# Optimization experiments

Measured on AMD Instinct MI355X. Metric: run time of the kernel, lower is better.

Reference implementation:

```python
import jax, jax.numpy as jnp
import numpy as np

B, H, W, C = 8, 56, 56, 384
HEADS = 12
HD = C // HEADS          # 32 head dim
WS = 7                   # window size
SS = 3                   # shift size
N = WS * WS              # 49 tokens per window
HID = int(C * 4.0)       # 1536 mlp hidden
NW = (H // WS) * (W // WS)  # 64 windows per image
EPS = 1e-5


def _relative_position_index(ws):
    coords = np.stack(np.meshgrid(np.arange(ws), np.arange(ws), indexing='ij'))
    cf = coords.reshape(2, -1)
    rel = (cf[:, :, None] - cf[:, None, :]).transpose(1, 2, 0)
    rel[:, :, 0] += ws - 1
    rel[:, :, 1] += ws - 1
    rel[:, :, 0] *= 2 * ws - 1
    return rel.sum(-1).astype(np.int32)  # [N, N]

REL_IDX = _relative_position_index(WS)


def _swin_shift_mask(hh, ww, ws, ss):
    # standard Swin shift mask: label 9 regions, windows with mixed labels get -100
    img = np.zeros((hh, ww), dtype=np.float32)
    cnt = 0
    for hs in (slice(0, -ws), slice(-ws, -ss), slice(-ss, None)):
        for wsl in (slice(0, -ws), slice(-ws, -ss), slice(-ss, None)):
            img[hs, wsl] = cnt
            cnt += 1
    wins = img.reshape(hh // ws, ws, ww // ws, ws).transpose(0, 2, 1, 3).reshape(-1, ws * ws)
    diff = wins[:, None, :] - wins[:, :, None]
    return np.where(diff != 0, -100.0, 0.0).astype(np.float32)  # [nW, N, N]


def setup_inputs() -> dict:
    key = jax.random.key(0)
    ks = jax.random.split(key, 8)
    s = 0.02
    return {
        'x': jax.random.normal(ks[0], (B, H, W, C), jnp.float32),
        'attention_mask': jnp.asarray(_swin_shift_mask(H, W, WS, SS)),
        'qkv_w': jax.random.normal(ks[1], (C, 3 * C), jnp.float32) * s,
        'qkv_b': jnp.zeros((3 * C,), jnp.float32),
        'proj_w': jax.random.normal(ks[2], (C, C), jnp.float32) * s,
        'proj_b': jnp.zeros((C,), jnp.float32),
        'rpb_table': jax.random.normal(ks[3], ((2 * WS - 1) * (2 * WS - 1), HEADS), jnp.float32) * s,
        'norm1_g': jnp.ones((C,), jnp.float32),
        'norm1_b': jnp.zeros((C,), jnp.float32),
        'norm2_g': jnp.ones((C,), jnp.float32),
        'norm2_b': jnp.zeros((C,), jnp.float32),
        'fc1_w': jax.random.normal(ks[4], (C, HID), jnp.float32) * s,
        'fc1_b': jnp.zeros((HID,), jnp.float32),
        'fc2_w': jax.random.normal(ks[5], (HID, C), jnp.float32) * s,
        'fc2_b': jnp.zeros((C,), jnp.float32),
    }


def _ln(x, g, b):
    mu = jnp.mean(x, axis=-1, keepdims=True)
    var = jnp.mean(jnp.square(x - mu), axis=-1, keepdims=True)
    return (x - mu) / jnp.sqrt(var + EPS) * g + b


def reference(x, attention_mask, qkv_w, qkv_b, proj_w, proj_b, rpb_table,
              norm1_g, norm1_b, norm2_g, norm2_b, fc1_w, fc1_b, fc2_w, fc2_b):
    b = x.shape[0]
    nh, nw = H // WS, W // WS
    shortcut = x.reshape(b, H * W, C)

    h = _ln(x, norm1_g, norm1_b)
    # cyclic shift (H,W divisible by WS -> no padding needed)
    h = jnp.roll(h, (-SS, -SS), axis=(1, 2))
    # window partition -> [b*nW, N, C]
    win = h.reshape(b, nh, WS, nw, WS, C).transpose(0, 1, 3, 2, 4, 5).reshape(-1, N, C)

    qkv = (win @ qkv_w + qkv_b).reshape(-1, N, 3, HEADS, HD).transpose(2, 0, 3, 1, 4)
    q, k, v = qkv[0] * (HD ** -0.5), qkv[1], qkv[2]  # each [b*nW, heads, N, HD]

    attn = jnp.einsum('bhnd,bhmd->bhnm', q, k)  # [b*nW, heads, N, N]
    bias = rpb_table[REL_IDX.reshape(-1)].reshape(N, N, HEADS).transpose(2, 0, 1)
    attn = attn + bias[None]
    # additive shift mask per window
    attn = attn.reshape(b, NW, HEADS, N, N) + attention_mask[None, :, None]
    attn = jax.nn.softmax(attn.reshape(-1, HEADS, N, N), axis=-1)

    out = jnp.einsum('bhnm,bhmd->bhnd', attn, v).transpose(0, 2, 1, 3).reshape(-1, N, C)
    out = out @ proj_w + proj_b
    # window reverse
    out = out.reshape(b, nh, nw, WS, WS, C).transpose(0, 1, 3, 2, 4, 5).reshape(b, H, W, C)
    out = jnp.roll(out, (SS, SS), axis=(1, 2)).reshape(b, H * W, C)

    xr = shortcut + out
    m = _ln(xr.reshape(b, H * W, C), norm2_g, norm2_b)
    m = jax.nn.gelu(m @ fc1_w + fc1_b, approximate=False) @ fc2_w + fc2_b
    xr = xr + m
    return xr.reshape(b, H, W, C)
```

## Files before the change

### kernel.cpp

```cpp
#include <hip/hip_runtime.h>
#include <hip/hip_bf16.h>
#include <math.h>

#define BD 8
#define HH 56
#define WW 56
#define CC 384
#define HEADS 12
#define HD 32
#define WS 7
#define SS 3
#define NTOK 49
#define NWIN 64
#define TOKENS (BD*HH*WW)
#define HID 1536
#define TPI (HH*WW)

typedef __attribute__((ext_vector_type(8))) short bf16x8;
typedef __attribute__((ext_vector_type(4))) float f32x4;

__device__ __forceinline__ unsigned short f2bf(float f) {
    unsigned int u = __float_as_uint(f);
    unsigned int r = (u + 0x7FFFu + ((u >> 16) & 1u)) >> 16;
    return (unsigned short)r;
}
__device__ __forceinline__ unsigned short f2bf_fast(float v) {
    unsigned int w;
    asm("v_cvt_pk_bf16_f32 %0, %1, %2" : "=v"(w) : "v"(v), "v"(v));
    return (unsigned short)w;
}
__device__ __forceinline__ float bf2f(unsigned short h) {
    return __uint_as_float(((unsigned int)h) << 16);
}
__device__ __forceinline__ void gload16(const void* g, void* l) {
    __builtin_amdgcn_global_load_lds((const __attribute__((address_space(1))) unsigned int*)g,
                                     (__attribute__((address_space(3))) unsigned int*)l, 16, 0, 0);
}
__device__ __forceinline__ float fgelu(float x) {
    float x2 = x * x;
    float y  = x * fmaf(0.03567740814f, x2, 0.7978845608f);
    float e  = exp2f(y * 2.8853900818f);
    float r  = __builtin_amdgcn_rcpf(e + 1.0f);
    return x - x * r;
}
__device__ __forceinline__ int xcd_swz(int lid, int nwg) {
    int xcd = lid & 7, pos = lid >> 3;
    int q = nwg >> 3, r = nwg & 7;
    return (xcd < r ? xcd * (q + 1) : r * (q + 1) + (xcd - r) * q) + pos;
}

__global__ __launch_bounds__(256)
void wprep(const float* __restrict__ W, unsigned short* __restrict__ Th, int K, int N)
{
    __shared__ float t[32][33];
    int n0 = blockIdx.x * 32, k0 = blockIdx.y * 32;
    int c = threadIdx.x & 31, r = threadIdx.x >> 5;
    #pragma unroll
    for (int rr = 0; rr < 32; rr += 8)
        t[r + rr][c] = W[(size_t)(k0 + r + rr) * N + n0 + c];
    __syncthreads();
    #pragma unroll
    for (int rr = 0; rr < 32; rr += 8) {
        int i = r + rr;
        Th[(size_t)(n0 + i) * K + k0 + c] = f2bf(t[c][i]);
    }
}

__global__ __launch_bounds__(256)
void bias_prep(const float* __restrict__ rpb, float* __restrict__ Bias)
{
    int e = blockIdx.x * 256 + threadIdx.x;
    int wtq = e / 49152;
    int hr  = e - wtq * 49152;
    int h   = hr >> 12;
    int rem = hr & 4095;
    int jt = rem >> 10, it = (rem >> 8) & 3, lane = (rem >> 2) & 63, reg = rem & 3;
    int j = jt * 16 + ((lane >> 4) << 2) + reg;
    int i = it * 16 + (lane & 15);
    float val;
    if (j >= NTOK) val = -1e30f;
    else if (i >= NTOK) val = 0.0f;
    else {
        int ti = i / 7, tj = i - ti * 7, yj = j / 7, xj = j - yj * 7;
        float b = rpb[((ti - yj + 6) * 13 + (tj - xj + 6)) * HEADS + h];
        int wh7 = wtq >> 1, ww7 = wtq & 1;
        int lhi = wh7 ? (ti < 4 ? 1 : 2) : 0, lhj = wh7 ? (yj < 4 ? 1 : 2) : 0;
        int lwi = ww7 ? (tj < 4 ? 1 : 2) : 0, lwj = ww7 ? (xj < 4 ? 1 : 2) : 0;
        if (lhi != lhj || lwi != lwj) b -= 100.0f;
        val = b * 5.65685424949238f;
    }
    Bias[e] = val;
}

template<bool SHIFT>
__global__ __launch_bounds__(128)
void ln_kernel(const float* __restrict__ in, const float* __restrict__ g,
               const float* __restrict__ beta, unsigned short* __restrict__ oh)
{
    int m = blockIdx.x;
    const float* src;
    size_t dbase = (size_t)m * CC;
    if (SHIFT) {
        int b  = m / (NWIN * NTOK);
        int rr = m % (NWIN * NTOK);
        int w  = rr / NTOK;
        int t  = rr % NTOK;
        int wh = w >> 3, ww = w & 7;
        int ti = t / 7,  tj = t - (t / 7) * 7;
        int hh = wh * WS + ti + SS;  if (hh >= HH) hh -= HH;
        int w2 = ww * WS + tj + SS;  if (w2 >= WW) w2 -= WW;
        src = in + ((size_t)b * TPI + hh * WW + w2) * CC;
    } else {
        src = in + (size_t)m * CC;
    }
    int tid = threadIdx.x;
    float v0 = src[tid], v1 = src[tid + 128], v2 = src[tid + 256];
    float s  = v0 + v1 + v2;
    float ss = v0*v0 + v1*v1 + v2*v2;
    #pragma unroll
    for (int off = 32; off > 0; off >>= 1) {
        s  += __shfl_down(s, off);
        ss += __shfl_down(ss, off);
    }
    __shared__ float red[4];
    int wid = tid >> 6, lane = tid & 63;
    if (lane == 0) { red[wid] = s; red[wid + 2] = ss; }
    __syncthreads();
    float tot   = red[0] + red[1];
    float totss = red[2] + red[3];
    float mu   = tot * (1.0f / CC);
    float var  = totss * (1.0f / CC) - mu * mu;
    float rstd = rsqrtf(var + 1e-5f);
    #pragma unroll
    for (int e = 0; e < 3; ++e) {
        int idx = tid + e * 128;
        float v = (e == 0 ? v0 : (e == 1 ? v1 : v2));
        float y = (v - mu) * rstd * g[idx] + beta[idx];
        oh[dbase + idx] = f2bf_fast(y);
    }
}

#define EPI_QKV  0
#define EPI_GELU 1
#define EPI_PROJ 2
#define EPI_FC2  3

#define COMPUTE128(B) do {                                                          \
    bf16x8 ah[4], bh[2];                                                            \
    _Pragma("unroll")                                                               \
    for (int f = 0; f < 4; ++f) {                                                   \
        int row = wr * 64 + f * 16 + rA;                                            \
        int pp = (kslot ^ ((row >> 1) & 3)) * 8;                                    \
        ah[f] = *(const bf16x8*)&lds[B][0][row][pp];                                \
    }                                                                               \
    _Pragma("unroll")                                                               \
    for (int f = 0; f < 2; ++f) {                                                   \
        int col = wc * 32 + f * 16 + rA;                                            \
        int pb = (kslot ^ ((col >> 1) & 3)) * 8;                                    \
        bh[f] = *(const bf16x8*)&lds[B][1][col][pb];                                \
    }                                                                               \
    _Pragma("unroll")                                                               \
    for (int i = 0; i < 4; ++i)                                                     \
        _Pragma("unroll")                                                           \
        for (int j = 0; j < 2; ++j)                                                 \
            acc[i][j] = __builtin_amdgcn_mfma_f32_16x16x32_bf16(ah[i], bh[j], acc[i][j], 0, 0, 0); \
} while (0)

template<int EPI>
__global__ __launch_bounds__(512)
void gemm_mfma(const unsigned short* __restrict__ Ah, const unsigned short* __restrict__ Bh,
               const float* __restrict__ bias, const float* __restrict__ extra,
               float* __restrict__ outf, unsigned short* __restrict__ outh,
               int M, int N, int K)
{
    __shared__ unsigned short lds[3][2][128][32];

    int nwg = gridDim.x * gridDim.y;
    int wid = xcd_swz(blockIdx.y * gridDim.x + blockIdx.x, nwg);
    int nblk = wid % gridDim.x;
    int mblk = wid / gridDim.x;

    int tid  = threadIdx.x;
    int lane = tid & 63;
    int wave = tid >> 6;
    int wr = wave >> 2;
    int wc = wave & 3;
    int m0 = mblk * 128, n0 = nblk * 128;

    int lrow = lane >> 2;
    int ps   = lane & 3;
    int kslot = lane >> 4;
    int rA    = lane & 15;

    const unsigned short* gsrc[2];
    unsigned short* d0[2];
    unsigned short* d1[2];
    unsigned short* d2[2];
    #pragma unroll
    for (int s = 0; s < 2; ++s) {
        int seg = wave * 2 + s;
        int bf = seg >> 3, c = seg & 7;
        const unsigned short* gb = (bf == 0) ? Ah : Bh;
        int r0 = (bf == 0) ? m0 : n0;
        int row = c * 16 + lrow;
        int ks = ps ^ ((row >> 1) & 3);
        gsrc[s] = gb + (size_t)(r0 + row) * K + ks * 8;
        d0[s] = &lds[0][bf][c * 16][0];
        d1[s] = &lds[1][bf][c * 16][0];
        d2[s] = &lds[2][bf][c * 16][0];
    }

    f32x4 acc[4][2];
    #pragma unroll
    for (int i = 0; i < 4; ++i)
        #pragma unroll
        for (int j = 0; j < 2; ++j)
            acc[i][j] = (f32x4){0.f, 0.f, 0.f, 0.f};

    const int nt = K / 32;
    gload16(gsrc[0], d0[0]);
    gload16(gsrc[1], d0[1]);
    gload16(gsrc[0] + 32, d1[0]);
    gload16(gsrc[1] + 32, d1[1]);
    for (int t = 0; t < nt; t += 3) {
        if (t + 2 < nt) {
            int ka = (t + 2) * 32;
            gload16(gsrc[0] + ka, d2[0]);
            gload16(gsrc[1] + ka, d2[1]);
            asm volatile("s_waitcnt vmcnt(4)" ::: "memory");
        } else if (t + 1 < nt) {
            asm volatile("s_waitcnt vmcnt(2)" ::: "memory");
        } else {
            asm volatile("s_waitcnt vmcnt(0)" ::: "memory");
        }
        __builtin_amdgcn_sched_barrier(0);
        __builtin_amdgcn_s_barrier();
        __builtin_amdgcn_sched_barrier(0);
        COMPUTE128(0);
        __builtin_amdgcn_s_barrier();
        if (t + 3 < nt) {
            int kb = (t + 3) * 32;
            gload16(gsrc[0] + kb, d0[0]);
            gload16(gsrc[1] + kb, d0[1]);
            asm volatile("s_waitcnt vmcnt(4)" ::: "memory");
        } else if (t + 2 < nt) {
            asm volatile("s_waitcnt vmcnt(2)" ::: "memory");
        } else {
            asm volatile("s_waitcnt vmcnt(0)" ::: "memory");
        }
        __builtin_amdgcn_sched_barrier(0);
        __builtin_amdgcn_s_barrier();
        __builtin_amdgcn_sched_barrier(0);
        COMPUTE128(1);
        __builtin_amdgcn_s_barrier();
        if (t + 4 < nt) {
            int kc = (t + 4) * 32;
            gload16(gsrc[0] + kc, d1[0]);
            gload16(gsrc[1] + kc, d1[1]);
            asm volatile("s_waitcnt vmcnt(4)" ::: "memory");
        } else if (t + 3 < nt) {
            asm volatile("s_waitcnt vmcnt(2)" ::: "memory");
        } else {
            asm volatile("s_waitcnt vmcnt(0)" ::: "memory");
        }
        __builtin_amdgcn_sched_barrier(0);
        __builtin_amdgcn_s_barrier();
        __builtin_amdgcn_sched_barrier(0);
        COMPUTE128(2);
        __builtin_amdgcn_s_barrier();
    }

    int cn = lane & 15;
    int rb = (lane >> 4) * 4;
    float bj[2];
    #pragma unroll
    for (int j = 0; j < 2; ++j) bj[j] = bias[n0 + wc * 32 + j * 16 + cn];
    int ncol = n0 + wc * 32 + cn;

    #pragma unroll
    for (int i = 0; i < 4; ++i) {
        #pragma unroll
        for (int r = 0; r < 4; ++r) {
            int mg = m0 + wr * 64 + i * 16 + rb + r;
            if (EPI == EPI_PROJ) {
                int b  = mg / (NWIN * NTOK);
                int rr = mg % (NWIN * NTOK);
                int w  = rr / NTOK;
                int t  = rr % NTOK;
                int wh = w >> 3, ww = w & 7;
                int ti = t / 7,  tj = t - (t / 7) * 7;
                int hh = wh * WS + ti + SS;  if (hh >= HH) hh -= HH;
                int w2 = ww * WS + tj + SS;  if (w2 >= WW) w2 -= WW;
                size_t pix = (size_t)b * TPI + hh * WW + w2;
                const float* xin = extra + pix * CC + ncol;
                float* xo = outf + pix * CC + ncol;
                #pragma unroll
                for (int j = 0; j < 2; ++j) xo[j * 16] = xin[j * 16] + acc[i][j][r] + bj[j];
            } else {
                const float* xi = extra + (size_t)mg * N + ncol;
                float* xo = outf + (size_t)mg * N + ncol;
                #pragma unroll
                for (int j = 0; j < 2; ++j) xo[j * 16] = xi[j * 16] + acc[i][j][r] + bj[j];
            }
        }
    }
}

#define COMPUTE256(B) do {                                                          \
    bf16x8 ah[4], bh[4];                                                            \
    _Pragma("unroll")                                                               \
    for (int f = 0; f < 4; ++f) {                                                   \
        int row = wr * 64 + f * 16 + rA;                                            \
        int pp = (kslot ^ ((row >> 1) & 3)) * 8;                                    \
        ah[f] = *(const bf16x8*)&ldsA[B][row][pp];                                  \
        int col = wc * 64 + f * 16 + rA;                                            \
        int pb = (kslot ^ ((col >> 1) & 3)) * 8;                                    \
        bh[f] = *(const bf16x8*)&ldsB[B][col][pb];                                  \
    }                                                                               \
    _Pragma("unroll")                                                               \
    for (int i = 0; i < 4; ++i)                                                     \
        _Pragma("unroll")                                                           \
        for (int j = 0; j < 4; ++j)                                                 \
            acc[i][j] = __builtin_amdgcn_mfma_f32_16x16x32_bf16(ah[i], bh[j], acc[i][j], 0, 0, 0); \
} while (0)

template<int EPI>
__global__ __launch_bounds__(512)
void gemm_mfma256(const unsigned short* __restrict__ Ah, const unsigned short* __restrict__ Bh,
                  const float* __restrict__ bias,
                  float* __restrict__ outf, unsigned short* __restrict__ outh,
                  int M, int N, int K)
{
    __shared__ unsigned short ldsA[2][256][32];
    __shared__ unsigned short ldsB[2][128][32];

    int nwg = gridDim.x * gridDim.y;
    int wid = xcd_swz(blockIdx.y * gridDim.x + blockIdx.x, nwg);
    int nblk = wid % gridDim.x;
    int mblk = wid / gridDim.x;

    int tid  = threadIdx.x;
    int lane = tid & 63;
    int wave = tid >> 6;
    int wr = wave >> 1;
    int wc = wave & 1;
    int m0 = mblk * 256, n0 = nblk * 128;

    int lrow = lane >> 2;
    int ps   = lane & 3;
    int kslot = lane >> 4;
    int rA    = lane & 15;

    const unsigned short* gsrc[3];
    unsigned short* d0[3];
    unsigned short* d1[3];
    #pragma unroll
    for (int s = 0; s < 3; ++s) {
        int seg = wave * 3 + s;
        const unsigned short* gb;
        unsigned short *l0, *l1;
        int c, r0;
        if (seg < 16) { gb = Ah; c = seg;      r0 = m0; l0 = &ldsA[0][c * 16][0]; l1 = &ldsA[1][c * 16][0]; }
        else          { gb = Bh; c = seg - 16; r0 = n0; l0 = &ldsB[0][c * 16][0]; l1 = &ldsB[1][c * 16][0]; }
        int row = c * 16 + lrow;
        int ks = ps ^ ((row >> 1) & 3);
        gsrc[s] = gb + (size_t)(r0 + row) * K + ks * 8;
        d0[s] = l0; d1[s] = l1;
    }

    f32x4 acc[4][4];
    #pragma unroll
    for (int i = 0; i < 4; ++i)
        #pragma unroll
        for (int j = 0; j < 4; ++j)
            acc[i][j] = (f32x4){0.f, 0.f, 0.f, 0.f};

    const int nt = K / 32;
    #pragma unroll
    for (int s = 0; s < 3; ++s) gload16(gsrc[s], d0[s]);
    for (int t = 0; t < nt; t += 2) {
        {
            int k1 = (t + 1) * 32;
            #pragma unroll
            for (int s = 0; s < 3; ++s) gload16(gsrc[s] + k1, d1[s]);
        }
        asm volatile("s_waitcnt vmcnt(3)" ::: "memory");
        __builtin_amdgcn_sched_barrier(0);
        __builtin_amdgcn_s_barrier();
        __builtin_amdgcn_sched_barrier(0);
        COMPUTE256(0);
        __builtin_amdgcn_s_barrier();
        if (t + 2 < nt) {
            int k2 = (t + 2) * 32;
            #pragma unroll
            for (int s = 0; s < 3; ++s) gload16(gsrc[s] + k2, d0[s]);
            asm volatile("s_waitcnt vmcnt(3)" ::: "memory");
        } else {
            asm volatile("s_waitcnt vmcnt(0)" ::: "memory");
        }
        __builtin_amdgcn_sched_barrier(0);
        __builtin_amdgcn_s_barrier();
        __builtin_amdgcn_sched_barrier(0);
        COMPUTE256(1);
        __builtin_amdgcn_s_barrier();
    }

    int cn = lane & 15;
    int rb = (lane >> 4) * 4;
    float bj[4];
    #pragma unroll
    for (int j = 0; j < 4; ++j) bj[j] = bias[n0 + wc * 64 + j * 16 + cn];
    int ncol = n0 + wc * 64 + cn;

    #pragma unroll
    for (int i = 0; i < 4; ++i) {
        #pragma unroll
        for (int r = 0; r < 4; ++r) {
            int mg = m0 + wr * 64 + i * 16 + rb + r;
            if (EPI == EPI_QKV) {
                unsigned short* orow = outh + (size_t)mg * N + ncol;
                #pragma unroll
                for (int j = 0; j < 4; ++j) orow[j * 16] = f2bf_fast(acc[i][j][r] + bj[j]);
            } else {
                unsigned short* orow = outh + (size_t)mg * N + ncol;
                #pragma unroll
                for (int j = 0; j < 4; ++j)
                    orow[j * 16] = f2bf_fast(fgelu(acc[i][j][r] + bj[j]));
            }
        }
    }
}

__global__ __launch_bounds__(256)
void attn3(const unsigned short* __restrict__ QKVb, const float* __restrict__ Bias,
           unsigned short* __restrict__ outh, int win0)
{
    int wave = threadIdx.x >> 6, lane = threadIdx.x & 63;
    int unit = blockIdx.x * 4 + wave;
    int head = unit % HEADS;
    int winl = unit / HEADS;
    int wing = win0 + winl;
    int wl   = wing & (NWIN - 1);
    int wt   = (((wl >> 3) == 7) << 1) | ((wl & 7) == 7);
    int qbase = winl * NTOK;
    size_t obase = (size_t)wing * NTOK;

    __shared__ __align__(16) unsigned short Pl_all[4][64][64];
    __shared__ __align__(16) unsigned short Vt_all[4][2048];
    unsigned short (*Pl)[64] = Pl_all[wave];
    unsigned short* Vt = Vt_all[wave];

    int l15 = lane & 15, g = lane >> 4;

    for (int idx = lane; idx < 480; idx += 64) {
        int d = idx & 31, t = 49 + (idx >> 5);
        Vt[d * 64 + (((t >> 3) ^ (d & 7)) << 3) + (t & 7)] = 0;
    }
    for (int idx = lane; idx < 196; idx += 64) {
        int t = idx >> 2, c = idx & 3;
        bf16x8 v = *(const bf16x8*)(QKVb + (size_t)(qbase + t) * 1152 + 768 + head * HD + c * 8);
        int tb = t >> 3, tl = t & 7;
        #pragma unroll
        for (int e = 0; e < 8; ++e) {
            int d = c * 8 + e;
            Vt[d * 64 + ((tb ^ e) << 3) + tl] = (unsigned short)v[e];
        }
    }

    bf16x8 kf[4], qf[4];
    #pragma unroll
    for (int t = 0; t < 4; ++t) {
        int rr = t * 16 + l15; if (rr > NTOK - 1) rr = NTOK - 1;
        const unsigned short* base = QKVb + (size_t)(qbase + rr) * 1152 + head * HD + g * 8;
        qf[t] = *(const bf16x8*)base;
        kf[t] = *(const bf16x8*)(base + 384);
    }

    const float* bb = Bias + (((size_t)wt * HEADS + head) << 12);
    f32x4 acc[4][4];
    #pragma unroll
    for (int jt = 0; jt < 4; ++jt)
        #pragma unroll
        for (int it = 0; it < 4; ++it) {
            f32x4 c = *(const f32x4*)(bb + ((jt * 4 + it) * 64 + lane) * 4);
            acc[jt][it] = __builtin_amdgcn_mfma_f32_16x16x32_bf16(kf[jt], qf[it], c, 0, 0, 0);
        }

    const float K1 = 0.25503488f;
    #pragma unroll
    for (int jt = 0; jt < 4; ++jt)
        #pragma unroll
        for (int it = 0; it < 4; ++it)
            #pragma unroll
            for (int r = 0; r < 4; ++r)
                acc[jt][it][r] = exp2f(acc[jt][it][r] * K1);

    #pragma unroll
    for (int it = 0; it < 4; ++it) {
        float s = 0.0f;
        #pragma unroll
        for (int jt = 0; jt < 4; ++jt)
            s += (acc[jt][it][0] + acc[jt][it][1]) + (acc[jt][it][2] + acc[jt][it][3]);
        s += __shfl_xor(s, 16);
        s += __shfl_xor(s, 32);
        float inv = 1.0f / s;
        int i  = it * 16 + l15;
        int sw = (i & 7) << 3;
        #pragma unroll
        for (int jt = 0; jt < 4; ++jt) {
            float a0 = acc[jt][it][0] * inv, a1 = acc[jt][it][1] * inv;
            float a2 = acc[jt][it][2] * inv, a3 = acc[jt][it][3] * inv;
            unsigned int w0, w1;
            asm("v_cvt_pk_bf16_f32 %0, %1, %2" : "=v"(w0) : "v"(a0), "v"(a1));
            asm("v_cvt_pk_bf16_f32 %0, %1, %2" : "=v"(w1) : "v"(a2), "v"(a3));
            int js = (jt * 16 + g * 4) ^ sw;
            *(unsigned int*)&Pl[i][js]     = w0;
            *(unsigned int*)&Pl[i][js + 2] = w1;
        }
    }

    bf16x8 vf[2][2];
    #pragma unroll
    for (int dt = 0; dt < 2; ++dt)
        #pragma unroll
        for (int kc = 0; kc < 2; ++kc) {
            int d = dt * 16 + l15;
            vf[dt][kc] = *(const bf16x8*)&Vt[d * 64 + (((kc * 4 + g) ^ (d & 7)) << 3)];
        }
    f32x4 oacc[4][2];
    #pragma unroll
    for (int it = 0; it < 4; ++it)
        #pragma unroll
        for (int dt = 0; dt < 2; ++dt)
            oacc[it][dt] = (f32x4){0.f, 0.f, 0.f, 0.f};

    #pragma unroll
    for (int it = 0; it < 4; ++it) {
        int i  = it * 16 + l15;
        int sw = (i & 7) << 3;
        #pragma unroll
        for (int kc = 0; kc < 2; ++kc) {
            int js = (kc * 32 + g * 8) ^ sw;
            bf16x8 pf = *(const bf16x8*)&Pl[i][js];
            #pragma unroll
            for (int dt = 0; dt < 2; ++dt)
                oacc[it][dt] = __builtin_amdgcn_mfma_f32_16x16x32_bf16(pf, vf[dt][kc], oacc[it][dt], 0, 0, 0);
        }
    }

    #pragma unroll
    for (int it = 0; it < 4; ++it) {
        #pragma unroll
        for (int r = 0; r < 4; ++r) {
            int i = it * 16 + g * 4 + r;
            if (i < NTOK) {
                unsigned short* orow = outh + (obase + i) * CC + head * HD;
                orow[l15]      = f2bf_fast(oacc[it][0][r]);
                orow[16 + l15] = f2bf_fast(oacc[it][1][r]);
            }
        }
    }
}

extern "C" void kernel_launch(void* const* d_in, const int* in_sizes, int n_in,
                              void* d_out, int out_size, void* d_ws, size_t ws_size,
                              hipStream_t stream)
{
    const float* x      = (const float*)d_in[0];
    const float* qkv_w  = (const float*)d_in[2];
    const float* qkv_b  = (const float*)d_in[3];
    const float* proj_w = (const float*)d_in[4];
    const float* proj_b = (const float*)d_in[5];
    const float* rpb    = (const float*)d_in[6];
    const float* n1g    = (const float*)d_in[7];
    const float* n1b    = (const float*)d_in[8];
    const float* n2g    = (const float*)d_in[9];
    const float* n2b    = (const float*)d_in[10];
    const float* fc1w   = (const float*)d_in[11];
    const float* fc1b   = (const float*)d_in[12];
    const float* fc2w   = (const float*)d_in[13];
    const float* fc2b   = (const float*)d_in[14];

    float* xr = (float*)d_out;

    unsigned short* p = (unsigned short*)d_ws;
    unsigned short* Wqh = p; p += 442368;
    unsigned short* Wph = p; p += 147456;
    unsigned short* W1h = p; p += 589824;
    unsigned short* W2h = p; p += 589824;
    unsigned short* ABh = p; p += (size_t)TOKENS * CC;
    float* Bias = (float*)p;
    unsigned short* region = (unsigned short*)(Bias + 196608);
    unsigned short* Hbuf = region;

    const size_t FIXED = 23592960;
    size_t R = (ws_size > FIXED) ? ws_size - FIXED : 0;
    int gq = 2;
    if (R >= (size_t)8 * TPI * 1152 * 2)      gq = 8;
    else if (R >= (size_t)4 * TPI * 1152 * 2) gq = 4;
    int gh = 2;
    if (R >= (size_t)8 * TPI * HID * 2)      gh = 8;
    else if (R >= (size_t)4 * TPI * HID * 2) gh = 4;

    unsigned short* QKVb = region;

    bias_prep<<<768, 256, 0, stream>>>(rpb, Bias);
    wprep<<<dim3(1152/32, 384/32), 256, 0, stream>>>(qkv_w, Wqh, 384, 1152);
    wprep<<<dim3(384/32,  384/32), 256, 0, stream>>>(proj_w, Wph, 384, 384);
    wprep<<<dim3(1536/32, 384/32), 256, 0, stream>>>(fc1w,  W1h, 384, 1536);
    wprep<<<dim3(384/32, 1536/32), 256, 0, stream>>>(fc2w,  W2h, 1536, 384);

    ln_kernel<true><<<TOKENS, 128, 0, stream>>>(x, n1g, n1b, ABh);

    for (int c = 0; c < 8 / gq; ++c) {
        size_t off = (size_t)c * gq * TPI;
        int M = gq * TPI;
        dim3 gmm((3 * CC) / 128, M / 256);
        gemm_mfma256<EPI_QKV><<<gmm, 512, 0, stream>>>(
            ABh + off * CC, Wqh, qkv_b, nullptr, QKVb, M, 3 * CC, CC);
        attn3<<<gq * NWIN * HEADS / 4, 256, 0, stream>>>(
            QKVb, Bias, ABh, c * gq * NWIN);
    }

    {
        dim3 gmm(CC / 128, TOKENS / 128);
        gemm_mfma<EPI_PROJ><<<gmm, 512, 0, stream>>>(
            ABh, Wph, proj_b, x, xr, nullptr, TOKENS, CC, CC);
    }

    ln_kernel<false><<<TOKENS, 128, 0, stream>>>(xr, n2g, n2b, ABh);

    for (int c = 0; c < 8 / gh; ++c) {
        size_t off = (size_t)c * gh * TPI;
        int M = gh * TPI;
        {
            dim3 gmm(HID / 128, M / 256);
            gemm_mfma256<EPI_GELU><<<gmm, 512, 0, stream>>>(
                ABh + off * CC, W1h, fc1b, nullptr, Hbuf, M, HID, CC);
        }
        {
            dim3 gmm(CC / 128, M / 128);
            gemm_mfma<EPI_FC2><<<gmm, 512, 0, stream>>>(
                Hbuf, W2h, fc2b, xr + off * CC, (float*)d_out + off * CC, nullptr, M, CC, HID);
        }
    }
}
```

Baseline: 211.2 us.

## Triple-buffer LDS tiles in MFMA GEMM to deepen global-load prefetch

The bf16 MFMA GEMM's shared-memory staging goes from two buffers to three, and the K loop is unrolled by three. Each iteration now keeps two tiles of global loads in flight (vmcnt(6)) while computing on the third, with tail-aware wait counts. The aim is to hide more global-memory latency behind MFMA work. In exchange, LDS use per block rises by half, which can lower the number of resident blocks per CU.

Result: no change. 212.0 us (+0.4%).

```diff
diff --git a/kernel.cpp b/kernel.cpp
--- a/kernel.cpp
+++ b/kernel.cpp
@@ -331,8 +331,8 @@
                   float* __restrict__ outf, unsigned short* __restrict__ outh,
                   int M, int N, int K)
 {
-    __shared__ unsigned short ldsA[2][256][32];
-    __shared__ unsigned short ldsB[2][128][32];
+    __shared__ unsigned short ldsA[3][256][32];
+    __shared__ unsigned short ldsB[3][128][32];
 
     int nwg = gridDim.x * gridDim.y;
     int wid = xcd_swz(blockIdx.y * gridDim.x + blockIdx.x, nwg);
@@ -354,18 +354,19 @@
     const unsigned short* gsrc[3];
     unsigned short* d0[3];
     unsigned short* d1[3];
+    unsigned short* d2[3];
     #pragma unroll
     for (int s = 0; s < 3; ++s) {
         int seg = wave * 3 + s;
         const unsigned short* gb;
-        unsigned short *l0, *l1;
+        unsigned short *l0, *l1, *l2;
         int c, r0;
-        if (seg < 16) { gb = Ah; c = seg;      r0 = m0; l0 = &ldsA[0][c * 16][0]; l1 = &ldsA[1][c * 16][0]; }
-        else          { gb = Bh; c = seg - 16; r0 = n0; l0 = &ldsB[0][c * 16][0]; l1 = &ldsB[1][c * 16][0]; }
+        if (seg < 16) { gb = Ah; c = seg;      r0 = m0; l0 = &ldsA[0][c * 16][0]; l1 = &ldsA[1][c * 16][0]; l2 = &ldsA[2][c * 16][0]; }
+        else          { gb = Bh; c = seg - 16; r0 = n0; l0 = &ldsB[0][c * 16][0]; l1 = &ldsB[1][c * 16][0]; l2 = &ldsB[2][c * 16][0]; }
         int row = c * 16 + lrow;
         int ks = ps ^ ((row >> 1) & 3);
         gsrc[s] = gb + (size_t)(r0 + row) * K + ks * 8;
-        d0[s] = l0; d1[s] = l1;
+        d0[s] = l0; d1[s] = l1; d2[s] = l2;
     }
 
     f32x4 acc[4][4];
@@ -378,22 +379,15 @@
     const int nt = K / 32;
     #pragma unroll
     for (int s = 0; s < 3; ++s) gload16(gsrc[s], d0[s]);
-    for (int t = 0; t < nt; t += 2) {
-        {
-            int k1 = (t + 1) * 32;
+    #pragma unroll
+    for (int s = 0; s < 3; ++s) gload16(gsrc[s] + 32, d1[s]);
+    for (int t = 0; t < nt; t += 3) {
+        if (t + 2 < nt) {
+            int ka = (t + 2) * 32;
             #pragma unroll
-            for (int s = 0; s < 3; ++s) gload16(gsrc[s] + k1, d1[s]);
-        }
-        asm volatile("s_waitcnt vmcnt(3)" ::: "memory");
-        __builtin_amdgcn_sched_barrier(0);
-        __builtin_amdgcn_s_barrier();
-        __builtin_amdgcn_sched_barrier(0);
-        COMPUTE256(0);
-        __builtin_amdgcn_s_barrier();
-        if (t + 2 < nt) {
-            int k2 = (t + 2) * 32;
-            #pragma unroll
-            for (int s = 0; s < 3; ++s) gload16(gsrc[s] + k2, d0[s]);
+            for (int s = 0; s < 3; ++s) gload16(gsrc[s] + ka, d2[s]);
+            asm volatile("s_waitcnt vmcnt(6)" ::: "memory");
+        } else if (t + 1 < nt) {
             asm volatile("s_waitcnt vmcnt(3)" ::: "memory");
         } else {
             asm volatile("s_waitcnt vmcnt(0)" ::: "memory");
@@ -401,7 +395,37 @@
         __builtin_amdgcn_sched_barrier(0);
         __builtin_amdgcn_s_barrier();
         __builtin_amdgcn_sched_barrier(0);
+        COMPUTE256(0);
+        __builtin_amdgcn_s_barrier();
+        if (t + 3 < nt) {
+            int kb = (t + 3) * 32;
+            #pragma unroll
+            for (int s = 0; s < 3; ++s) gload16(gsrc[s] + kb, d0[s]);
+            asm volatile("s_waitcnt vmcnt(6)" ::: "memory");
+        } else if (t + 2 < nt) {
+            asm volatile("s_waitcnt vmcnt(3)" ::: "memory");
+        } else {
+            asm volatile("s_waitcnt vmcnt(0)" ::: "memory");
+        }
+        __builtin_amdgcn_sched_barrier(0);
+        __builtin_amdgcn_s_barrier();
+        __builtin_amdgcn_sched_barrier(0);
         COMPUTE256(1);
+        __builtin_amdgcn_s_barrier();
+        if (t + 4 < nt) {
+            int kc = (t + 4) * 32;
+            #pragma unroll
+            for (int s = 0; s < 3; ++s) gload16(gsrc[s] + kc, d1[s]);
+            asm volatile("s_waitcnt vmcnt(6)" ::: "memory");
+        } else if (t + 3 < nt) {
+            asm volatile("s_waitcnt vmcnt(3)" ::: "memory");
+        } else {
+            asm volatile("s_waitcnt vmcnt(0)" ::: "memory");
+        }
+        __builtin_amdgcn_sched_barrier(0);
+        __builtin_amdgcn_s_barrier();
+        __builtin_amdgcn_sched_barrier(0);
+        COMPUTE256(2);
         __builtin_amdgcn_s_barrier();
     }
 
```
